# Kernel tuning notes

Measured on AMD Instinct MI355X. Metric: run time of the kernel, lower is better.

The kernel has to match this reference:

```python
import jax, jax.numpy as jnp
import numpy as np

N = 50000          # atoms (nodes)
NEIGH = 12         # neighbors per atom
N_CRYS = 500       # crystals, 100 atoms each (contiguous)
H_E = 128          # h_fea_edge
H_A = 128          # h_fea_angle
N_CLS = 2
BOND_STEPS, BOND_MIN, BOND_MAX = 40, 0.0, 8.0
ANG_STEPS, ANG_MIN, ANG_MAX = 8, -1.0, 1.0


def _gbf(data, dmin, dmax, steps):
    # Gaussian basis expansion on the last (new) axis
    filters = jnp.linspace(dmin, dmax, steps, dtype=jnp.float32)
    gamma = (dmax - dmin) / steps
    return jnp.exp(-((data[..., None] - filters) ** 2) / (gamma ** 2))


def _sage_conv(x, src, dst, Wl, Wr, b):
    # PyG SAGEConv, mean aggregation:
    #   out_i = Wl @ mean_{(j->i) in E} x_j + b + Wr @ x_i
    n = x.shape[0]
    msg = x[src]                                             # [E, F] gather
    agg = jax.ops.segment_sum(msg, dst, num_segments=n)      # [N, F] scatter-add
    cnt = jax.ops.segment_sum(jnp.ones((src.shape[0],), x.dtype), dst, num_segments=n)
    agg = agg / jnp.maximum(cnt, 1.0)[:, None]
    return agg @ Wl.T + b + x @ Wr.T


def _segment_mean_pool(x, crys_idx):
    # crys_idx: [C, 2] contiguous [start, end) ranges covering [0, N)
    n = x.shape[0]
    starts = crys_idx[:, 0]
    seg_id = jnp.searchsorted(starts, jnp.arange(n), side='right') - 1
    counts = (crys_idx[:, 1] - crys_idx[:, 0]).astype(x.dtype)
    summed = jax.ops.segment_sum(x, seg_id, num_segments=crys_idx.shape[0])
    return summed / jnp.maximum(counts, 1.0)[:, None]


def setup_inputs() -> dict:
    key = jax.random.key(0)
    ks = jax.random.split(key, 24)
    in_b = BOND_STEPS * NEIGH            # 480
    in_a = ANG_STEPS * NEIGH * NEIGH     # 1152
    h_cat = H_E + H_A                    # 256

    def lin(k, fo, fi):
        return jax.random.normal(k, (fo, fi), jnp.float32) * (1.0 / np.sqrt(fi))

    atoms_per = N // N_CRYS
    starts = np.arange(N_CRYS, dtype=np.int32) * atoms_per
    crys_idx = jnp.asarray(np.stack([starts, starts + atoms_per], axis=1))

    return {
        'bond_fea': jax.random.uniform(ks[0], (N, NEIGH), jnp.float32) * BOND_MAX,
        'angle_fea': jax.random.uniform(ks[1], (N, NEIGH, NEIGH), jnp.float32) * 2.0 - 1.0,
        'species': jax.random.randint(ks[2], (N,), 0, 100, jnp.int32),
        'nbr_idx': jax.random.randint(ks[3], (N, NEIGH), 0, N, jnp.int32),
        'crys_idx': crys_idx,
        'Wl_b1': lin(ks[4], H_E, in_b), 'Wr_b1': lin(ks[5], H_E, in_b),
        'b_b1': jnp.zeros((H_E,), jnp.float32),
        'Wl_a1': lin(ks[6], H_A, in_a), 'Wr_a1': lin(ks[7], H_A, in_a),
        'b_a1': jnp.zeros((H_A,), jnp.float32),
        'Wl_b': jnp.stack([lin(ks[8], H_E, H_E), lin(ks[9], H_E, H_E)]),
        'Wr_b': jnp.stack([lin(ks[10], H_E, H_E), lin(ks[11], H_E, H_E)]),
        'b_b': jnp.zeros((2, H_E), jnp.float32),
        'Wl_a': jnp.stack([lin(ks[12], H_A, H_A), lin(ks[13], H_A, H_A)]),
        'Wr_a': jnp.stack([lin(ks[14], H_A, H_A), lin(ks[15], H_A, H_A)]),
        'b_a': jnp.zeros((2, H_A), jnp.float32),
        'W_mlp': jnp.stack([lin(ks[16], h_cat, h_cat), lin(ks[17], h_cat, h_cat)]),
        'b_mlp': jnp.zeros((2, h_cat), jnp.float32),
        'W_fc': lin(ks[18], N_CLS, h_cat),
        'b_fc': jnp.zeros((N_CLS,), jnp.float32),
    }


def reference(bond_fea, angle_fea, species, nbr_idx, crys_idx,
              Wl_b1, Wr_b1, b_b1, Wl_a1, Wr_a1, b_a1,
              Wl_b, Wr_b, b_b, Wl_a, Wr_a, b_a,
              W_mlp, b_mlp, W_fc, b_fc):
    n, neigh = nbr_idx.shape
    # get_edge_index: source = repeated node id, dest = neighbor id
    src = jnp.repeat(jnp.arange(n, dtype=nbr_idx.dtype), neigh)   # [N*neigh]
    dst = nbr_idx.reshape(-1)                                     # [N*neigh]

    # GBF expansions, flattened per node
    edge_fea = _gbf(bond_fea, BOND_MIN, BOND_MAX, BOND_STEPS).reshape(n, -1)    # [N, 480]
    ang_fea = _gbf(angle_fea, ANG_MIN, ANG_MAX, ANG_STEPS).reshape(n, -1)       # [N, 1152]

    # first SAGE layers (dropout_prob = 0 -> identity)
    b_out = jax.nn.relu(_sage_conv(edge_fea, src, dst, Wl_b1, Wr_b1, b_b1))
    a_out = jax.nn.relu(_sage_conv(ang_fea, src, dst, Wl_a1, Wr_a1, b_a1))

    # stacked SAGE layers (n_conv - 1 = 2 each)
    for i in range(Wl_b.shape[0]):
        b_out = jax.nn.relu(_sage_conv(b_out, src, dst, Wl_b[i], Wr_b[i], b_b[i]))
    for i in range(Wl_a.shape[0]):
        a_out = jax.nn.relu(_sage_conv(a_out, src, dst, Wl_a[i], Wr_a[i], b_a[i]))

    crys_fea = jnp.concatenate([b_out, a_out], axis=1)   # [N, 256]
    crys_fea = _segment_mean_pool(crys_fea, crys_idx)     # [C, 256]

    for i in range(W_mlp.shape[0]):
        crys_fea = crys_fea @ W_mlp[i].T + b_mlp[i]

    return crys_fea @ W_fc.T + b_fc                       # [C, n_classification]
```

## Files before the change

kernel.cpp:

```cpp
#include <hip/hip_runtime.h>

typedef _Float16 f16;
typedef _Float16 f16x8 __attribute__((ext_vector_type(8)));
typedef float f32x4 __attribute__((ext_vector_type(4)));

#define N_ATOMS 50000
#define NEIGH   12
#define NEDGE   (N_ATOMS * NEIGH)
#define NCRYS   500
#define NBLK    196

__device__ __forceinline__ void gld_lds16(const void* g, void* l) {
  __builtin_amdgcn_global_load_lds(
      (const __attribute__((address_space(1))) unsigned int*)g,
      (__attribute__((address_space(3))) unsigned int*)l, 16, 0, 0);
}

template <int MODE, int K>
__global__ __launch_bounds__(512) void gemm16(
    const void* __restrict__ Asrc, const f16* __restrict__ Wcat,
    f16* __restrict__ P, f16* __restrict__ Q, int n) {
  __shared__ __align__(16) f16 As[2][4][128][8];
  __shared__ __align__(16) f16 Bs[2][4][256][8];
  const int tid = threadIdx.x;
  const int lane = tid & 63;
  const int wid = tid >> 6;
  const int wr = wid >> 2;
  const int wc = wid & 3;
  const int row0 = blockIdx.x * 128;

  const int sArow = tid & 127;
  const int sAkb = tid >> 7;
  const int sBcol = tid & 255;
  const int sBkb = tid >> 8;

  int arow = row0 + sArow;
  if (arow >= n) arow = n - 1;

  f32x4 acc[4][4];
#pragma unroll
  for (int m = 0; m < 4; ++m)
#pragma unroll
    for (int q = 0; q < 4; ++q) acc[m][q] = (f32x4)0.f;

  auto stage = [&](int buf, int k0) {
#pragma unroll
    for (int p = 0; p < 2; ++p) {
      int kb = sBkb + 2 * p;
      gld_lds16(Wcat + (size_t)sBcol * K + k0 + kb * 8, &Bs[buf][kb][sBcol][0]);
    }
    if constexpr (MODE == 0) {
      gld_lds16((const f16*)Asrc + (size_t)arow * K + k0 + sAkb * 8,
                &As[buf][sAkb][sArow][0]);
    } else {
      f16 v[8];
#pragma unroll
      for (int j = 0; j < 8; ++j) {
        int kg = k0 + sAkb * 8 + j;
        float d, f, g2i;
        if constexpr (MODE == 1) {
          int jn = kg / 40;
          int kk = kg - jn * 40;
          d = ((const float*)Asrc)[arow * NEIGH + jn];
          f = kk * (8.0f / 39.0f);
          g2i = 25.0f;
        } else {
          int jn = kg >> 3;
          int kk = kg & 7;
          d = ((const float*)Asrc)[arow * 144 + jn];
          f = -1.0f + kk * (2.0f / 7.0f);
          g2i = 16.0f;
        }
        float t = d - f;
        v[j] = (f16)__expf(-t * t * g2i);
      }
      *(f16x8*)&As[buf][sAkb][sArow][0] = *(const f16x8*)v;
    }
  };

  constexpr int NT = K / 32;
  stage(0, 0);
  __syncthreads();
  int buf = 0;
  for (int t = 0; t < NT; ++t) {
    if (t + 1 < NT) stage(buf ^ 1, (t + 1) * 32);
    const int kb = lane >> 4;
    const int r16 = lane & 15;
    f16x8 a[4], b[4];
#pragma unroll
    for (int m = 0; m < 4; ++m)
      a[m] = *(const f16x8*)&As[buf][kb][wr * 64 + m * 16 + r16][0];
#pragma unroll
    for (int q = 0; q < 4; ++q)
      b[q] = *(const f16x8*)&Bs[buf][kb][wc * 64 + q * 16 + r16][0];
#pragma unroll
    for (int m = 0; m < 4; ++m)
#pragma unroll
      for (int q = 0; q < 4; ++q)
        acc[m][q] =
            __builtin_amdgcn_mfma_f32_16x16x32_f16(a[m], b[q], acc[m][q], 0, 0, 0);
    __syncthreads();
    buf ^= 1;
  }

  const int crow = (lane >> 4) * 4;
  const int ccol = lane & 15;
  f16* baseo = (wc < 2) ? P : Q;
  const int cbase = (wc & 1) * 64;
#pragma unroll
  for (int m = 0; m < 4; ++m) {
#pragma unroll
    for (int r = 0; r < 4; ++r) {
      int row = row0 + wr * 64 + m * 16 + crow + r;
      if (row < n) {
#pragma unroll
        for (int q = 0; q < 4; ++q) {
          int col = cbase + q * 16 + ccol;
          baseo[(size_t)row * 128 + col] = (f16)acc[m][q][r];
        }
      }
    }
  }
}

__global__ void cvtW(const float* __restrict__ Wl, const float* __restrict__ Wr,
                     f16* __restrict__ outp, int K) {
  int c = blockIdx.y;
  int k = blockIdx.x * 256 + threadIdx.x;
  if (k < K)
    outp[(size_t)c * K + k] =
        (f16)((c < 128) ? Wl[(size_t)c * K + k] : Wr[(size_t)(c - 128) * K + k]);
}

__global__ void cvtW_small(const float* __restrict__ Wl_b, const float* __restrict__ Wr_b,
                           const float* __restrict__ Wl_a, const float* __restrict__ Wr_a,
                           f16* __restrict__ outp) {
  int idx = blockIdx.x * 256 + threadIdx.x;
  int l = idx >> 15;
  int c = (idx >> 7) & 255;
  int k = idx & 127;
  const float* Wl = (l < 2) ? Wl_b + (size_t)l * 16384 : Wl_a + (size_t)(l - 2) * 16384;
  const float* Wr = (l < 2) ? Wr_b + (size_t)l * 16384 : Wr_a + (size_t)(l - 2) * 16384;
  float v = (c < 128) ? Wl[(size_t)c * 128 + k] : Wr[(size_t)(c - 128) * 128 + k];
  outp[idx] = (f16)v;
}

__global__ void k_count(const int* __restrict__ nbr, int* __restrict__ deg) {
  int e = blockIdx.x * 256 + threadIdx.x;
  if (e < NEDGE) atomicAdd(&deg[nbr[e]], 1);
}

__global__ void k_scan1(const int* __restrict__ deg, int* __restrict__ rowptr,
                        int* __restrict__ bsum) {
  __shared__ int s[256];
  int t = threadIdx.x, i = blockIdx.x * 256 + t;
  int v = (i < N_ATOMS) ? deg[i] : 0;
  s[t] = v;
  __syncthreads();
  for (int off = 1; off < 256; off <<= 1) {
    int x = (t >= off) ? s[t - off] : 0;
    __syncthreads();
    s[t] += x;
    __syncthreads();
  }
  if (i < N_ATOMS) rowptr[i] = s[t] - v;
  if (t == 255) bsum[blockIdx.x] = s[255];
}

__global__ void k_scan2(int* __restrict__ bsum) {
  __shared__ int s[256];
  int t = threadIdx.x;
  int v = (t < NBLK) ? bsum[t] : 0;
  s[t] = v;
  __syncthreads();
  for (int off = 1; off < 256; off <<= 1) {
    int x = (t >= off) ? s[t - off] : 0;
    __syncthreads();
    s[t] += x;
    __syncthreads();
  }
  if (t < NBLK) bsum[t] = s[t] - v;
}

__global__ void k_scan3(int* __restrict__ rowptr, const int* __restrict__ bsum) {
  int i = blockIdx.x * 256 + threadIdx.x;
  if (i < N_ATOMS) rowptr[i] += bsum[blockIdx.x];
  if (i == 0) rowptr[N_ATOMS] = NEDGE;
}

__global__ void k_fill(const int* __restrict__ nbr, const int* __restrict__ rowptr,
                       int* __restrict__ cursor, int* __restrict__ eidx) {
  int e = blockIdx.x * 256 + threadIdx.x;
  if (e < NEDGE) {
    int dst = nbr[e];
    int pos = rowptr[dst] + atomicAdd(&cursor[dst], 1);
    eidx[pos] = e / NEIGH;
  }
}

__global__ __launch_bounds__(256) void gather_fin(
    const f16* __restrict__ P, const f16* __restrict__ Q,
    const int* __restrict__ rowptr, const int* __restrict__ eidx,
    const float* __restrict__ bias, f16* __restrict__ x) {
  const int t = threadIdx.x;
  const int a = blockIdx.x * 16 + (t >> 4);
  const int g = (t & 15) * 8;
  const int s0 = rowptr[a], s1 = rowptr[a + 1];
  float acc[8];
#pragma unroll
  for (int u = 0; u < 8; ++u) acc[u] = 0.f;
  int j = s0;
  for (; j + 4 <= s1; j += 4) {
    int src0 = eidx[j], src1 = eidx[j + 1], src2 = eidx[j + 2], src3 = eidx[j + 3];
    f16x8 v0 = *(const f16x8*)&P[(size_t)src0 * 128 + g];
    f16x8 v1 = *(const f16x8*)&P[(size_t)src1 * 128 + g];
    f16x8 v2 = *(const f16x8*)&P[(size_t)src2 * 128 + g];
    f16x8 v3 = *(const f16x8*)&P[(size_t)src3 * 128 + g];
#pragma unroll
    for (int u = 0; u < 8; ++u)
      acc[u] += ((float)v0[u] + (float)v1[u]) + ((float)v2[u] + (float)v3[u]);
  }
  for (; j < s1; ++j) {
    f16x8 v = *(const f16x8*)&P[(size_t)eidx[j] * 128 + g];
#pragma unroll
    for (int u = 0; u < 8; ++u) acc[u] += (float)v[u];
  }
  f16x8 q = *(const f16x8*)&Q[(size_t)a * 128 + g];
  float4 b0 = *(const float4*)(bias + g);
  float4 b1 = *(const float4*)(bias + g + 4);
  float bb[8] = {b0.x, b0.y, b0.z, b0.w, b1.x, b1.y, b1.z, b1.w};
  float inv = 1.0f / fmaxf((float)(s1 - s0), 1.0f);
  f16 outv[8];
#pragma unroll
  for (int u = 0; u < 8; ++u) {
    float v = acc[u] * inv + bb[u] + (float)q[u];
    outv[u] = (f16)fmaxf(v, 0.0f);
  }
  *(f16x8*)&x[(size_t)a * 128 + g] = *(const f16x8*)outv;
}

__global__ __launch_bounds__(256) void head_kernel(
    const f16* __restrict__ xb, const f16* __restrict__ xa,
    const int* __restrict__ crys, const float* __restrict__ W_mlp,
    const float* __restrict__ b_mlp, const float* __restrict__ W_fc,
    const float* __restrict__ b_fc, float* __restrict__ outp) {
  __shared__ float sh0[256], sh1[256];
  const int cry = blockIdx.x, c = threadIdx.x;
  const int s = crys[2 * cry], e = crys[2 * cry + 1];
  const f16* src = (c < 128) ? xb : xa;
  const int ch = c & 127;
  float sum = 0.f;
  for (int r = s; r < e; ++r) sum += (float)src[(size_t)r * 128 + ch];
  sh0[c] = sum / fmaxf((float)(e - s), 1.0f);
  __syncthreads();
  {
    const float* wrow = W_mlp + (size_t)c * 256;
    float s2 = b_mlp[c];
#pragma unroll 8
    for (int k = 0; k < 256; k += 4) {
      float4 w = *(const float4*)&wrow[k];
      s2 += sh0[k] * w.x + sh0[k + 1] * w.y + sh0[k + 2] * w.z + sh0[k + 3] * w.w;
    }
    sh1[c] = s2;
  }
  __syncthreads();
  {
    const float* wrow = W_mlp + 65536 + (size_t)c * 256;
    float s2 = b_mlp[256 + c];
#pragma unroll 8
    for (int k = 0; k < 256; k += 4) {
      float4 w = *(const float4*)&wrow[k];
      s2 += sh1[k] * w.x + sh1[k + 1] * w.y + sh1[k + 2] * w.z + sh1[k + 3] * w.w;
    }
    sh0[c] = s2;
  }
  __syncthreads();
  if (c < 2) {
    const float* wrow = W_fc + c * 256;
    float s2 = b_fc[c];
    for (int k = 0; k < 256; ++k) s2 += sh0[k] * wrow[k];
    outp[cry * 2 + c] = s2;
  }
}

extern "C" void kernel_launch(void* const* d_in, const int* in_sizes, int n_in,
                              void* d_out, int out_size, void* d_ws, size_t ws_size,
                              hipStream_t stream) {
  const float* bond  = (const float*)d_in[0];
  const float* angle = (const float*)d_in[1];
  const int*   nbr   = (const int*)d_in[3];
  const int*   crys  = (const int*)d_in[4];
  const float* Wl_b1 = (const float*)d_in[5];
  const float* Wr_b1 = (const float*)d_in[6];
  const float* b_b1  = (const float*)d_in[7];
  const float* Wl_a1 = (const float*)d_in[8];
  const float* Wr_a1 = (const float*)d_in[9];
  const float* b_a1  = (const float*)d_in[10];
  const float* Wl_b  = (const float*)d_in[11];
  const float* Wr_b  = (const float*)d_in[12];
  const float* b_b   = (const float*)d_in[13];
  const float* Wl_a  = (const float*)d_in[14];
  const float* Wr_a  = (const float*)d_in[15];
  const float* b_a   = (const float*)d_in[16];
  const float* W_mlp = (const float*)d_in[17];
  const float* b_mlp = (const float*)d_in[18];
  const float* W_fc  = (const float*)d_in[19];
  const float* b_fc  = (const float*)d_in[20];

  char* w = (char*)d_ws;
  auto alloc = [&](size_t bytes) {
    void* p = (void*)w;
    w += (bytes + 15) & ~(size_t)15;
    return p;
  };
  f16* P16    = (f16*)alloc((size_t)N_ATOMS * 128 * 2);
  f16* Q16    = (f16*)alloc((size_t)N_ATOMS * 128 * 2);
  f16* xb16   = (f16*)alloc((size_t)N_ATOMS * 128 * 2);
  f16* xa16   = (f16*)alloc((size_t)N_ATOMS * 128 * 2);
  f16* Wb1c   = (f16*)alloc((size_t)256 * 480 * 2);
  f16* Wa1c   = (f16*)alloc((size_t)256 * 1152 * 2);
  f16* Wsm    = (f16*)alloc((size_t)4 * 256 * 128 * 2);
  int* deg    = (int*)alloc((size_t)N_ATOMS * 4);
  int* cursor = (int*)alloc((size_t)N_ATOMS * 4);
  int* rowptr = (int*)alloc((size_t)(N_ATOMS + 1) * 4);
  int* eidx   = (int*)alloc((size_t)NEDGE * 4);
  int* bsum   = (int*)alloc(256 * 4);

  cvtW<<<dim3(2, 256), 256, 0, stream>>>(Wl_b1, Wr_b1, Wb1c, 480);
  cvtW<<<dim3(5, 256), 256, 0, stream>>>(Wl_a1, Wr_a1, Wa1c, 1152);
  cvtW_small<<<512, 256, 0, stream>>>(Wl_b, Wr_b, Wl_a, Wr_a, Wsm);

  hipMemsetAsync(deg, 0, (size_t)2 * N_ATOMS * 4, stream);
  k_count<<<(NEDGE + 255) / 256, 256, 0, stream>>>(nbr, deg);
  k_scan1<<<NBLK, 256, 0, stream>>>(deg, rowptr, bsum);
  k_scan2<<<1, 256, 0, stream>>>(bsum);
  k_scan3<<<NBLK, 256, 0, stream>>>(rowptr, bsum);
  k_fill<<<(NEDGE + 255) / 256, 256, 0, stream>>>(nbr, rowptr, cursor, eidx);

  const int GG = (N_ATOMS + 127) / 128;
  const int AG = N_ATOMS / 16;

  gemm16<1, 480><<<GG, 512, 0, stream>>>(bond, Wb1c, P16, Q16, N_ATOMS);
  gather_fin<<<AG, 256, 0, stream>>>(P16, Q16, rowptr, eidx, b_b1, xb16);
  for (int l = 0; l < 2; ++l) {
    gemm16<0, 128><<<GG, 512, 0, stream>>>(xb16, Wsm + (size_t)l * 32768, P16, Q16, N_ATOMS);
    gather_fin<<<AG, 256, 0, stream>>>(P16, Q16, rowptr, eidx, b_b + l * 128, xb16);
  }

  gemm16<2, 1152><<<GG, 512, 0, stream>>>(angle, Wa1c, P16, Q16, N_ATOMS);
  gather_fin<<<AG, 256, 0, stream>>>(P16, Q16, rowptr, eidx, b_a1, xa16);
  for (int l = 0; l < 2; ++l) {
    gemm16<0, 128><<<GG, 512, 0, stream>>>(xa16, Wsm + (size_t)(2 + l) * 32768, P16, Q16, N_ATOMS);
    gather_fin<<<AG, 256, 0, stream>>>(P16, Q16, rowptr, eidx, b_a + l * 128, xa16);
  }

  head_kernel<<<NCRYS, 256, 0, stream>>>(xb16, xa16, crys, W_mlp, b_mlp, W_fc, b_fc,
                                         (float*)d_out);
}
```

Baseline: 449.0 us.

## Aggregate-then-transform for 128-wide SAGE layers and batch bond/angle paths

For the 128-wide layers, the mean is now gathered first into a concatenated [mean | x] buffer. A single K=256 GEMM then applies bias and ReLU in its epilogue, replacing the GEMM-to-P/Q then gather_fin sequence. Bond and angle branches run in the same launches via blockIdx.y, and the first-layer GEMM uses 64-row tiles with the GBF computed once per 8-element chunk. This removes the intermediate P/Q writes and halves launch count, but the gather now reads and writes a wider 256-stride buffer and there are more small-tile GEMM blocks.

```diff
diff --git a/kernel.cpp b/kernel.cpp
--- a/kernel.cpp
+++ b/kernel.cpp
@@ -17,29 +17,28 @@
 }
 
 template <int MODE, int K>
-__global__ __launch_bounds__(512) void gemm16(
-    const void* __restrict__ Asrc, const f16* __restrict__ Wcat,
+__global__ __launch_bounds__(512) void gemm1(
+    const float* __restrict__ Asrc, const f16* __restrict__ Wcat,
     f16* __restrict__ P, f16* __restrict__ Q, int n) {
-  __shared__ __align__(16) f16 As[2][4][128][8];
+  __shared__ __align__(16) f16 As[2][4][64][8];
   __shared__ __align__(16) f16 Bs[2][4][256][8];
   const int tid = threadIdx.x;
   const int lane = tid & 63;
   const int wid = tid >> 6;
   const int wr = wid >> 2;
   const int wc = wid & 3;
-  const int row0 = blockIdx.x * 128;
-
-  const int sArow = tid & 127;
-  const int sAkb = tid >> 7;
+  const int row0 = blockIdx.x * 64;
+
   const int sBcol = tid & 255;
   const int sBkb = tid >> 8;
-
+  const int sArow = tid & 63;
+  const int sAkb = (tid >> 6) & 3;
   int arow = row0 + sArow;
   if (arow >= n) arow = n - 1;
 
-  f32x4 acc[4][4];
-#pragma unroll
-  for (int m = 0; m < 4; ++m)
+  f32x4 acc[2][4];
+#pragma unroll
+  for (int m = 0; m < 2; ++m)
 #pragma unroll
     for (int q = 0; q < 4; ++q) acc[m][q] = (f32x4)0.f;
 
@@ -49,30 +48,26 @@
       int kb = sBkb + 2 * p;
       gld_lds16(Wcat + (size_t)sBcol * K + k0 + kb * 8, &Bs[buf][kb][sBcol][0]);
     }
-    if constexpr (MODE == 0) {
-      gld_lds16((const f16*)Asrc + (size_t)arow * K + k0 + sAkb * 8,
-                &As[buf][sAkb][sArow][0]);
-    } else {
+    if (tid < 256) {
+      int kg0 = k0 + sAkb * 8;
       f16 v[8];
-#pragma unroll
-      for (int j = 0; j < 8; ++j) {
-        int kg = k0 + sAkb * 8 + j;
-        float d, f, g2i;
-        if constexpr (MODE == 1) {
-          int jn = kg / 40;
-          int kk = kg - jn * 40;
-          d = ((const float*)Asrc)[arow * NEIGH + jn];
-          f = kk * (8.0f / 39.0f);
-          g2i = 25.0f;
-        } else {
-          int jn = kg >> 3;
-          int kk = kg & 7;
-          d = ((const float*)Asrc)[arow * 144 + jn];
-          f = -1.0f + kk * (2.0f / 7.0f);
-          g2i = 16.0f;
+      if constexpr (MODE == 1) {
+        int jn = kg0 / 40;
+        int kk0 = kg0 - jn * 40;
+        float d = Asrc[arow * NEIGH + jn];
+#pragma unroll
+        for (int j = 0; j < 8; ++j) {
+          float t = d - (kk0 + j) * (8.0f / 39.0f);
+          v[j] = (f16)__expf(-t * t * 25.0f);
         }
-        float t = d - f;
-        v[j] = (f16)__expf(-t * t * g2i);
+      } else {
+        int jn = kg0 >> 3;
+        float d = Asrc[arow * 144 + jn];
+#pragma unroll
+        for (int j = 0; j < 8; ++j) {
+          float t = d - (-1.0f + j * (2.0f / 7.0f));
+          v[j] = (f16)__expf(-t * t * 16.0f);
+        }
       }
       *(f16x8*)&As[buf][sAkb][sArow][0] = *(const f16x8*)v;
     }
@@ -86,15 +81,15 @@
     if (t + 1 < NT) stage(buf ^ 1, (t + 1) * 32);
     const int kb = lane >> 4;
     const int r16 = lane & 15;
-    f16x8 a[4], b[4];
-#pragma unroll
-    for (int m = 0; m < 4; ++m)
-      a[m] = *(const f16x8*)&As[buf][kb][wr * 64 + m * 16 + r16][0];
+    f16x8 a[2], b[4];
+#pragma unroll
+    for (int m = 0; m < 2; ++m)
+      a[m] = *(const f16x8*)&As[buf][kb][wr * 32 + m * 16 + r16][0];
 #pragma unroll
     for (int q = 0; q < 4; ++q)
       b[q] = *(const f16x8*)&Bs[buf][kb][wc * 64 + q * 16 + r16][0];
 #pragma unroll
-    for (int m = 0; m < 4; ++m)
+    for (int m = 0; m < 2; ++m)
 #pragma unroll
       for (int q = 0; q < 4; ++q)
         acc[m][q] =
@@ -108,15 +103,95 @@
   f16* baseo = (wc < 2) ? P : Q;
   const int cbase = (wc & 1) * 64;
 #pragma unroll
-  for (int m = 0; m < 4; ++m) {
+  for (int m = 0; m < 2; ++m) {
 #pragma unroll
     for (int r = 0; r < 4; ++r) {
-      int row = row0 + wr * 64 + m * 16 + crow + r;
+      int row = row0 + wr * 32 + m * 16 + crow + r;
       if (row < n) {
 #pragma unroll
+        for (int q = 0; q < 4; ++q)
+          baseo[(size_t)row * 128 + cbase + q * 16 + ccol] = (f16)acc[m][q][r];
+      }
+    }
+  }
+}
+
+__global__ __launch_bounds__(256) void gemmL(
+    f16* __restrict__ axb, f16* __restrict__ axa, const f16* __restrict__ Wall,
+    const float* __restrict__ bb, const float* __restrict__ ba, int lidx, int n) {
+  __shared__ __align__(16) f16 As[2][4][64][8];
+  __shared__ __align__(16) f16 Bs[2][4][128][8];
+  const int path = blockIdx.y;
+  f16* ax = path ? axa : axb;
+  const f16* W = Wall + (size_t)(path * 2 + lidx) * 32768;
+  const float* bias = (path ? ba : bb) + lidx * 128;
+
+  const int tid = threadIdx.x;
+  const int lane = tid & 63;
+  const int wid = tid >> 6;
+  const int wr = wid >> 1;
+  const int wc = wid & 1;
+  const int row0 = blockIdx.x * 64;
+
+  const int sArow = tid & 63;
+  const int sAkb = tid >> 6;
+  int arow = row0 + sArow;
+  if (arow >= n) arow = n - 1;
+
+  f32x4 acc[2][4];
+#pragma unroll
+  for (int m = 0; m < 2; ++m)
+#pragma unroll
+    for (int q = 0; q < 4; ++q) acc[m][q] = (f32x4)0.f;
+
+  auto stage = [&](int buf, int k0) {
+#pragma unroll
+    for (int p = 0; p < 2; ++p) {
+      int u = p * 4 + wid;
+      int kb = u & 3;
+      int c = (u >> 2) * 64 + lane;
+      gld_lds16(W + (size_t)c * 256 + k0 + kb * 8, &Bs[buf][kb][c][0]);
+    }
+    gld_lds16(ax + (size_t)arow * 256 + k0 + sAkb * 8, &As[buf][sAkb][sArow][0]);
+  };
+
+  stage(0, 0);
+  __syncthreads();
+  int buf = 0;
+  for (int t = 0; t < 8; ++t) {
+    if (t + 1 < 8) stage(buf ^ 1, (t + 1) * 32);
+    const int kb = lane >> 4;
+    const int r16 = lane & 15;
+    f16x8 a[2], b[4];
+#pragma unroll
+    for (int m = 0; m < 2; ++m)
+      a[m] = *(const f16x8*)&As[buf][kb][wr * 32 + m * 16 + r16][0];
+#pragma unroll
+    for (int q = 0; q < 4; ++q)
+      b[q] = *(const f16x8*)&Bs[buf][kb][wc * 64 + q * 16 + r16][0];
+#pragma unroll
+    for (int m = 0; m < 2; ++m)
+#pragma unroll
+      for (int q = 0; q < 4; ++q)
+        acc[m][q] =
+            __builtin_amdgcn_mfma_f32_16x16x32_f16(a[m], b[q], acc[m][q], 0, 0, 0);
+    __syncthreads();
+    buf ^= 1;
+  }
+
+  const int crow = (lane >> 4) * 4;
+  const int ccol = lane & 15;
+#pragma unroll
+  for (int m = 0; m < 2; ++m) {
+#pragma unroll
+    for (int r = 0; r < 4; ++r) {
+      int row = row0 + wr * 32 + m * 16 + crow + r;
+      if (row < n) {
+#pragma unroll
         for (int q = 0; q < 4; ++q) {
-          int col = cbase + q * 16 + ccol;
-          baseo[(size_t)row * 128 + col] = (f16)acc[m][q][r];
+          int col = wc * 64 + q * 16 + ccol;
+          float v = acc[m][q][r] + bias[col];
+          ax[(size_t)row * 256 + 128 + col] = (f16)fmaxf(v, 0.0f);
         }
       }
     }
@@ -137,11 +212,11 @@
                            f16* __restrict__ outp) {
   int idx = blockIdx.x * 256 + threadIdx.x;
   int l = idx >> 15;
-  int c = (idx >> 7) & 255;
-  int k = idx & 127;
+  int c = (idx >> 8) & 127;
+  int k = idx & 255;
   const float* Wl = (l < 2) ? Wl_b + (size_t)l * 16384 : Wl_a + (size_t)(l - 2) * 16384;
   const float* Wr = (l < 2) ? Wr_b + (size_t)l * 16384 : Wr_a + (size_t)(l - 2) * 16384;
-  float v = (c < 128) ? Wl[(size_t)c * 128 + k] : Wr[(size_t)(c - 128) * 128 + k];
+  float v = (k < 128) ? Wl[(size_t)c * 128 + k] : Wr[(size_t)c * 128 + (k - 128)];
   outp[idx] = (f16)v;
 }
 
@@ -149,7 +224,6 @@
   int e = blockIdx.x * 256 + threadIdx.x;
   if (e < NEDGE) atomicAdd(&deg[nbr[e]], 1);
 }
-
 __global__ void k_scan1(const int* __restrict__ deg, int* __restrict__ rowptr,
                         int* __restrict__ bsum) {
   __shared__ int s[256];
@@ -166,7 +240,6 @@
   if (i < N_ATOMS) rowptr[i] = s[t] - v;
   if (t == 255) bsum[blockIdx.x] = s[255];
 }
-
 __global__ void k_scan2(int* __restrict__ bsum) {
   __shared__ int s[256];
   int t = threadIdx.x;
@@ -181,13 +254,11 @@
   }
   if (t < NBLK) bsum[t] = s[t] - v;
 }
-
 __global__ void k_scan3(int* __restrict__ rowptr, const int* __restrict__ bsum) {
   int i = blockIdx.x * 256 + threadIdx.x;
   if (i < N_ATOMS) rowptr[i] += bsum[blockIdx.x];
   if (i == 0) rowptr[N_ATOMS] = NEDGE;
 }
-
 __global__ void k_fill(const int* __restrict__ nbr, const int* __restrict__ rowptr,
                        int* __restrict__ cursor, int* __restrict__ eidx) {
   int e = blockIdx.x * 256 + threadIdx.x;
@@ -198,10 +269,17 @@
   }
 }
 
-__global__ __launch_bounds__(256) void gather_fin(
-    const f16* __restrict__ P, const f16* __restrict__ Q,
+__global__ __launch_bounds__(256) void gather_fin1(
+    const f16* __restrict__ Pb, const f16* __restrict__ Qb,
+    const f16* __restrict__ Pa, const f16* __restrict__ Qa,
     const int* __restrict__ rowptr, const int* __restrict__ eidx,
-    const float* __restrict__ bias, f16* __restrict__ x) {
+    const float* __restrict__ bias_b, const float* __restrict__ bias_a,
+    f16* __restrict__ axb, f16* __restrict__ axa) {
+  const int path = blockIdx.y;
+  const f16* P = path ? Pa : Pb;
+  const f16* Q = path ? Qa : Qb;
+  const float* bias = path ? bias_a : bias_b;
+  f16* ax = path ? axa : axb;
   const int t = threadIdx.x;
   const int a = blockIdx.x * 16 + (t >> 4);
   const int g = (t & 15) * 8;
@@ -226,31 +304,62 @@
     for (int u = 0; u < 8; ++u) acc[u] += (float)v[u];
   }
   f16x8 q = *(const f16x8*)&Q[(size_t)a * 128 + g];
-  float4 b0 = *(const float4*)(bias + g);
-  float4 b1 = *(const float4*)(bias + g + 4);
-  float bb[8] = {b0.x, b0.y, b0.z, b0.w, b1.x, b1.y, b1.z, b1.w};
   float inv = 1.0f / fmaxf((float)(s1 - s0), 1.0f);
   f16 outv[8];
 #pragma unroll
   for (int u = 0; u < 8; ++u) {
-    float v = acc[u] * inv + bb[u] + (float)q[u];
+    float v = acc[u] * inv + bias[g + u] + (float)q[u];
     outv[u] = (f16)fmaxf(v, 0.0f);
   }
-  *(f16x8*)&x[(size_t)a * 128 + g] = *(const f16x8*)outv;
+  *(f16x8*)&ax[(size_t)a * 256 + 128 + g] = *(const f16x8*)outv;
+}
+
+__global__ __launch_bounds__(256) void gather_mean(
+    f16* __restrict__ axb, f16* __restrict__ axa,
+    const int* __restrict__ rowptr, const int* __restrict__ eidx) {
+  f16* ax = blockIdx.y ? axa : axb;
+  const int t = threadIdx.x;
+  const int a = blockIdx.x * 16 + (t >> 4);
+  const int g = (t & 15) * 8;
+  const int s0 = rowptr[a], s1 = rowptr[a + 1];
+  float acc[8];
+#pragma unroll
+  for (int u = 0; u < 8; ++u) acc[u] = 0.f;
+  int j = s0;
+  for (; j + 4 <= s1; j += 4) {
+    int src0 = eidx[j], src1 = eidx[j + 1], src2 = eidx[j + 2], src3 = eidx[j + 3];
+    f16x8 v0 = *(const f16x8*)&ax[(size_t)src0 * 256 + 128 + g];
+    f16x8 v1 = *(const f16x8*)&ax[(size_t)src1 * 256 + 128 + g];
+    f16x8 v2 = *(const f16x8*)&ax[(size_t)src2 * 256 + 128 + g];
+    f16x8 v3 = *(const f16x8*)&ax[(size_t)src3 * 256 + 128 + g];
+#pragma unroll
+    for (int u = 0; u < 8; ++u)
+      acc[u] += ((float)v0[u] + (float)v1[u]) + ((float)v2[u] + (float)v3[u]);
+  }
+  for (; j < s1; ++j) {
+    f16x8 v = *(const f16x8*)&ax[(size_t)eidx[j] * 256 + 128 + g];
+#pragma unroll
+    for (int u = 0; u < 8; ++u) acc[u] += (float)v[u];
+  }
+  float inv = 1.0f / fmaxf((float)(s1 - s0), 1.0f);
+  f16 outv[8];
+#pragma unroll
+  for (int u = 0; u < 8; ++u) outv[u] = (f16)(acc[u] * inv);
+  *(f16x8*)&ax[(size_t)a * 256 + g] = *(const f16x8*)outv;
 }
 
 __global__ __launch_bounds__(256) void head_kernel(
-    const f16* __restrict__ xb, const f16* __restrict__ xa,
+    const f16* __restrict__ axb, const f16* __restrict__ axa,
     const int* __restrict__ crys, const float* __restrict__ W_mlp,
     const float* __restrict__ b_mlp, const float* __restrict__ W_fc,
     const float* __restrict__ b_fc, float* __restrict__ outp) {
   __shared__ float sh0[256], sh1[256];
   const int cry = blockIdx.x, c = threadIdx.x;
   const int s = crys[2 * cry], e = crys[2 * cry + 1];
-  const f16* src = (c < 128) ? xb : xa;
+  const f16* src = (c < 128) ? axb : axa;
   const int ch = c & 127;
   float sum = 0.f;
-  for (int r = s; r < e; ++r) sum += (float)src[(size_t)r * 128 + ch];
+  for (int r = s; r < e; ++r) sum += (float)src[(size_t)r * 256 + 128 + ch];
   sh0[c] = sum / fmaxf((float)(e - s), 1.0f);
   __syncthreads();
   {
@@ -310,18 +419,20 @@
   char* w = (char*)d_ws;
   auto alloc = [&](size_t bytes) {
     void* p = (void*)w;
-    w += (bytes + 15) & ~(size_t)15;
+    w += (bytes + 255) & ~(size_t)255;
     return p;
   };
-  f16* P16    = (f16*)alloc((size_t)N_ATOMS * 128 * 2);
-  f16* Q16    = (f16*)alloc((size_t)N_ATOMS * 128 * 2);
-  f16* xb16   = (f16*)alloc((size_t)N_ATOMS * 128 * 2);
-  f16* xa16   = (f16*)alloc((size_t)N_ATOMS * 128 * 2);
-  f16* Wb1c   = (f16*)alloc((size_t)256 * 480 * 2);
-  f16* Wa1c   = (f16*)alloc((size_t)256 * 1152 * 2);
-  f16* Wsm    = (f16*)alloc((size_t)4 * 256 * 128 * 2);
-  int* deg    = (int*)alloc((size_t)N_ATOMS * 4);
-  int* cursor = (int*)alloc((size_t)N_ATOMS * 4);
+  f16* Pb   = (f16*)alloc((size_t)N_ATOMS * 128 * 2);
+  f16* Qb   = (f16*)alloc((size_t)N_ATOMS * 128 * 2);
+  f16* Pa   = (f16*)alloc((size_t)N_ATOMS * 128 * 2);
+  f16* Qa   = (f16*)alloc((size_t)N_ATOMS * 128 * 2);
+  f16* axb  = (f16*)alloc((size_t)N_ATOMS * 256 * 2);
+  f16* axa  = (f16*)alloc((size_t)N_ATOMS * 256 * 2);
+  f16* Wb1c = (f16*)alloc((size_t)256 * 480 * 2);
+  f16* Wa1c = (f16*)alloc((size_t)256 * 1152 * 2);
+  f16* Wsm  = (f16*)alloc((size_t)4 * 128 * 256 * 2);
+  int* deg    = (int*)alloc((size_t)2 * N_ATOMS * 4);
+  int* cursor = deg + N_ATOMS;
   int* rowptr = (int*)alloc((size_t)(N_ATOMS + 1) * 4);
   int* eidx   = (int*)alloc((size_t)NEDGE * 4);
   int* bsum   = (int*)alloc(256 * 4);
@@ -337,23 +448,19 @@
   k_scan3<<<NBLK, 256, 0, stream>>>(rowptr, bsum);
   k_fill<<<(NEDGE + 255) / 256, 256, 0, stream>>>(nbr, rowptr, cursor, eidx);
 
-  const int GG = (N_ATOMS + 127) / 128;
+  const int GG = (N_ATOMS + 63) / 64;
   const int AG = N_ATOMS / 16;
 
-  gemm16<1, 480><<<GG, 512, 0, stream>>>(bond, Wb1c, P16, Q16, N_ATOMS);
-  gather_fin<<<AG, 256, 0, stream>>>(P16, Q16, rowptr, eidx, b_b1, xb16);
+  gemm1<1, 480><<<GG, 512, 0, stream>>>(bond, Wb1c, Pb, Qb, N_ATOMS);
+  gemm1<2, 1152><<<GG, 512, 0, stream>>>(angle, Wa1c, Pa, Qa, N_ATOMS);
+  gather_fin1<<<dim3(AG, 2), 256, 0, stream>>>(Pb, Qb, Pa, Qa, rowptr, eidx,
+                                               b_b1, b_a1, axb, axa);
+
   for (int l = 0; l < 2; ++l) {
-    gemm16<0, 128><<<GG, 512, 0, stream>>>(xb16, Wsm + (size_t)l * 32768, P16, Q16, N_ATOMS);
-    gather_fin<<<AG, 256, 0, stream>>>(P16, Q16, rowptr, eidx, b_b + l * 128, xb16);
-  }
-
-  gemm16<2, 1152><<<GG, 512, 0, stream>>>(angle, Wa1c, P16, Q16, N_ATOMS);
-  gather_fin<<<AG, 256, 0, stream>>>(P16, Q16, rowptr, eidx, b_a1, xa16);
-  for (int l = 0; l < 2; ++l) {
-    gemm16<0, 128><<<GG, 512, 0, stream>>>(xa16, Wsm + (size_t)(2 + l) * 32768, P16, Q16, N_ATOMS);
-    gather_fin<<<AG, 256, 0, stream>>>(P16, Q16, rowptr, eidx, b_a + l * 128, xa16);
-  }
-
-  head_kernel<<<NCRYS, 256, 0, stream>>>(xb16, xa16, crys, W_mlp, b_mlp, W_fc, b_fc,
+    gather_mean<<<dim3(AG, 2), 256, 0, stream>>>(axb, axa, rowptr, eidx);
+    gemmL<<<dim3(GG, 2), 256, 0, stream>>>(axb, axa, Wsm, b_b, b_a, l, N_ATOMS);
+  }
+
+  head_kernel<<<NCRYS, 256, 0, stream>>>(axb, axa, crys, W_mlp, b_mlp, W_fc, b_fc,
                                          (float*)d_out);
 }
```

After: 497.7 us. 1.11x slower.
